# Kernel tuning notes

Hardware: AMD Instinct MI355X
Metric: run time of the kernel (lower is better)

## Reference

```python
import jax, jax.numpy as jnp
import numpy as np

H = 4096   # hidden_dim
I = 4096   # input_dim
V = 32000  # output_size


def setup_inputs() -> dict:
    key = jax.random.key(0)
    ks = jax.random.split(key, 16)
    s_x = 1.0 / np.sqrt(I)
    s_h = 1.0 / np.sqrt(H)
    inp = {
        'prev_h': jax.random.normal(ks[0], (H,), jnp.float32),
        'prev_c': jax.random.normal(ks[1], (H,), jnp.float32),
        'x_t': jax.random.normal(ks[2], (I,), jnp.float32),
        'w_xf': jax.random.normal(ks[3], (H, I), jnp.float32) * s_x,
        'w_hf': jax.random.normal(ks[4], (H, H), jnp.float32) * s_h,
        'b_f': jnp.zeros((H,), jnp.float32),
        'w_xi': jax.random.normal(ks[5], (H, I), jnp.float32) * s_x,
        'w_hi': jax.random.normal(ks[6], (H, H), jnp.float32) * s_h,
        'b_i': jnp.zeros((H,), jnp.float32),
        'w_xg': jax.random.normal(ks[7], (H, I), jnp.float32) * s_x,
        'w_hg': jax.random.normal(ks[8], (H, H), jnp.float32) * s_h,
        'b_g': jnp.zeros((H,), jnp.float32),
        'w_xo': jax.random.normal(ks[9], (H, I), jnp.float32) * s_x,
        'w_ho': jax.random.normal(ks[10], (H, H), jnp.float32) * s_h,
        'b_o': jnp.zeros((H,), jnp.float32),
        'w_hy': jax.random.normal(ks[11], (V, H), jnp.float32) * s_h,
        'b_y': jnp.zeros((V,), jnp.float32),
    }
    return inp


def reference(prev_h, prev_c, x_t,
              w_xf, w_hf, b_f,
              w_xi, w_hi, b_i,
              w_xg, w_hg, b_g,
              w_xo, w_ho, b_o,
              w_hy, b_y):
    # Fuse the 8 small matvecs into 2 stacked matvecs: [4H, I] @ x and [4H, H] @ h.
    W_x = jnp.concatenate([w_xf, w_xi, w_xg, w_xo], axis=0)  # [4H, I]
    W_h = jnp.concatenate([w_hf, w_hi, w_hg, w_ho], axis=0)  # [4H, H]
    b = jnp.concatenate([b_f, b_i, b_g, b_o], axis=0)        # [4H]
    gates = W_x @ x_t + W_h @ prev_h + b                      # [4H]
    f_t = jax.nn.sigmoid(gates[0:H])
    i_t = jax.nn.sigmoid(gates[H:2 * H])
    g_t = jnp.tanh(gates[2 * H:3 * H])
    o_t = jax.nn.sigmoid(gates[3 * H:4 * H])
    c_t = f_t * prev_c + i_t * g_t
    h_t = o_t * jnp.tanh(c_t)
    y_t = jax.nn.softmax(w_hy @ h_t + b_y, axis=-1)           # [V]
    return (h_t, c_t, y_t)
```

## Files before the change

### kernel.cpp

```cpp
#include <hip/hip_runtime.h>
#include <math.h>

#define HDIM 4096
#define VDIM 32000
#define NPART 125

__device__ inline float wave_reduce_sum(float v) {
    #pragma unroll
    for (int off = 32; off > 0; off >>= 1)
        v += __shfl_down(v, off, 64);
    return v;
}

__device__ inline float wave_reduce_max(float v) {
    #pragma unroll
    for (int off = 32; off > 0; off >>= 1)
        v = fmaxf(v, __shfl_down(v, off, 64));
    return v;
}

__global__ __launch_bounds__(256) void lstm_gates_kernel(
    const float* __restrict__ prev_h, const float* __restrict__ prev_c,
    const float* __restrict__ x_t,
    const float* __restrict__ w_xf, const float* __restrict__ w_hf, const float* __restrict__ b_f,
    const float* __restrict__ w_xi, const float* __restrict__ w_hi, const float* __restrict__ b_i,
    const float* __restrict__ w_xg, const float* __restrict__ w_hg, const float* __restrict__ b_g,
    const float* __restrict__ w_xo, const float* __restrict__ w_ho, const float* __restrict__ b_o,
    float* __restrict__ out)
{
    __shared__ float s_x[HDIM];
    __shared__ float s_h[HDIM];
    for (int i = threadIdx.x * 4; i < HDIM; i += 256 * 4) {
        *reinterpret_cast<float4*>(&s_x[i]) = *reinterpret_cast<const float4*>(&x_t[i]);
        *reinterpret_cast<float4*>(&s_h[i]) = *reinterpret_cast<const float4*>(&prev_h[i]);
    }
    __syncthreads();

    const int row  = blockIdx.x;
    const int wave = threadIdx.x >> 6;
    const int lane = threadIdx.x & 63;

    const float* wx; const float* wh; const float* bb;
    if      (wave == 0) { wx = w_xf; wh = w_hf; bb = b_f; }
    else if (wave == 1) { wx = w_xi; wh = w_hi; bb = b_i; }
    else if (wave == 2) { wx = w_xg; wh = w_hg; bb = b_g; }
    else                { wx = w_xo; wh = w_ho; bb = b_o; }
    wx += (size_t)row * HDIM;
    wh += (size_t)row * HDIM;

    float accx = 0.f, acch = 0.f;
    #pragma unroll 4
    for (int j = lane * 4; j < HDIM; j += 64 * 4) {
        float4 a = *reinterpret_cast<const float4*>(wx + j);
        float4 v = *reinterpret_cast<const float4*>(&s_x[j]);
        accx += a.x * v.x + a.y * v.y + a.z * v.z + a.w * v.w;
        float4 b = *reinterpret_cast<const float4*>(wh + j);
        float4 u = *reinterpret_cast<const float4*>(&s_h[j]);
        acch += b.x * u.x + b.y * u.y + b.z * u.z + b.w * u.w;
    }
    float acc = wave_reduce_sum(accx + acch);

    __shared__ float g4[4];
    if (lane == 0) g4[wave] = acc + bb[row];
    __syncthreads();
    if (threadIdx.x == 0) {
        float ft = 1.f / (1.f + expf(-g4[0]));
        float it = 1.f / (1.f + expf(-g4[1]));
        float gt = tanhf(g4[2]);
        float ot = 1.f / (1.f + expf(-g4[3]));
        float c  = ft * prev_c[row] + it * gt;
        float h  = ot * tanhf(c);
        out[row]        = h;
        out[HDIM + row] = c;
    }
}

__global__ __launch_bounds__(256) void logits_kernel(
    const float* __restrict__ w_hy, const float* __restrict__ b_y,
    const float* __restrict__ h, float* __restrict__ logits)
{
    __shared__ float s_h[HDIM];
    for (int i = threadIdx.x * 4; i < HDIM; i += 256 * 4)
        *reinterpret_cast<float4*>(&s_h[i]) = *reinterpret_cast<const float4*>(&h[i]);
    __syncthreads();

    const int row  = blockIdx.x * 4 + (threadIdx.x >> 6);
    const int lane = threadIdx.x & 63;
    const float* w = w_hy + (size_t)row * HDIM;

    float acc0 = 0.f, acc1 = 0.f;
    #pragma unroll 4
    for (int j = lane * 8; j < HDIM; j += 64 * 8) {
        float4 a = *reinterpret_cast<const float4*>(w + j);
        float4 v = *reinterpret_cast<const float4*>(&s_h[j]);
        acc0 += a.x * v.x + a.y * v.y + a.z * v.z + a.w * v.w;
        float4 b = *reinterpret_cast<const float4*>(w + j + 4);
        float4 u = *reinterpret_cast<const float4*>(&s_h[j + 4]);
        acc1 += b.x * u.x + b.y * u.y + b.z * u.z + b.w * u.w;
    }
    float acc = wave_reduce_sum(acc0 + acc1);
    if (lane == 0) logits[row] = acc + b_y[row];
}

__global__ __launch_bounds__(256) void softmax_partial_kernel(
    const float* __restrict__ logits, float2* __restrict__ part)
{
    const int wave = threadIdx.x >> 6;
    const int lane = threadIdx.x & 63;
    float v = logits[blockIdx.x * 256 + threadIdx.x];

    float m = wave_reduce_max(v);
    __shared__ float sm[4];
    if (lane == 0) sm[wave] = m;
    __syncthreads();
    m = fmaxf(fmaxf(sm[0], sm[1]), fmaxf(sm[2], sm[3]));

    float s = wave_reduce_sum(expf(v - m));
    __shared__ float ss[4];
    if (lane == 0) ss[wave] = s;
    __syncthreads();
    if (threadIdx.x == 0)
        part[blockIdx.x] = make_float2(m, ss[0] + ss[1] + ss[2] + ss[3]);
}

__global__ __launch_bounds__(128) void softmax_combine_kernel(
    const float2* __restrict__ part, float* __restrict__ stats)
{
    const int tid = threadIdx.x;
    float2 p = (tid < NPART) ? part[tid] : make_float2(-1e30f, 0.f);

    float m = wave_reduce_max(p.x);
    __shared__ float sm[2];
    if ((tid & 63) == 0) sm[tid >> 6] = m;
    __syncthreads();
    float M = fmaxf(sm[0], sm[1]);

    float s = wave_reduce_sum(p.y * expf(p.x - M));
    __shared__ float s2[2];
    if ((tid & 63) == 0) s2[tid >> 6] = s;
    __syncthreads();
    if (tid == 0) { stats[0] = M; stats[1] = 1.f / (s2[0] + s2[1]); }
}

__global__ __launch_bounds__(256) void softmax_norm_kernel(
    const float* __restrict__ logits, const float* __restrict__ stats,
    float* __restrict__ y)
{
    const int i = blockIdx.x * 256 + threadIdx.x;
    if (i < VDIM) y[i] = expf(logits[i] - stats[0]) * stats[1];
}

extern "C" void kernel_launch(void* const* d_in, const int* in_sizes, int n_in,
                              void* d_out, int out_size, void* d_ws, size_t ws_size,
                              hipStream_t stream)
{
    const float* prev_h = (const float*)d_in[0];
    const float* prev_c = (const float*)d_in[1];
    const float* x_t    = (const float*)d_in[2];
    const float* w_xf   = (const float*)d_in[3];
    const float* w_hf   = (const float*)d_in[4];
    const float* b_f    = (const float*)d_in[5];
    const float* w_xi   = (const float*)d_in[6];
    const float* w_hi   = (const float*)d_in[7];
    const float* b_i    = (const float*)d_in[8];
    const float* w_xg   = (const float*)d_in[9];
    const float* w_hg   = (const float*)d_in[10];
    const float* b_g    = (const float*)d_in[11];
    const float* w_xo   = (const float*)d_in[12];
    const float* w_ho   = (const float*)d_in[13];
    const float* b_o    = (const float*)d_in[14];
    const float* w_hy   = (const float*)d_in[15];
    const float* b_y    = (const float*)d_in[16];

    float* out = (float*)d_out;
    float* h_t = out;
    float* y_t = out + 2 * HDIM;

    float*  logits = (float*)d_ws;
    float*  stats  = logits + VDIM;
    float2* part   = (float2*)(stats + 2);

    lstm_gates_kernel<<<HDIM, 256, 0, stream>>>(
        prev_h, prev_c, x_t,
        w_xf, w_hf, b_f, w_xi, w_hi, b_i,
        w_xg, w_hg, b_g, w_xo, w_ho, b_o, out);

    logits_kernel<<<VDIM / 4, 256, 0, stream>>>(w_hy, b_y, h_t, logits);

    softmax_partial_kernel<<<NPART, 256, 0, stream>>>(logits, part);

    softmax_combine_kernel<<<1, 128, 0, stream>>>(part, stats);

    softmax_norm_kernel<<<(VDIM + 255) / 256, 256, 0, stream>>>(logits, stats, y_t);
}
```

Before: 190.4 us.

## Process four rows per wave, fuse softmax partials into logits, use nontemporal loads

Both matvec kernels now have each wave compute four rows instead of one, so each shared-memory vector load is reused across four weight rows, and the block count drops accordingly. Weight loads use nontemporal hints because the matrices are streamed once. The per-block softmax max/sum partial is computed inside the logits kernel, which removes the separate partial kernel and its reread of the logits. The combine stage becomes one 1024-thread block using an online max/sum over 2000 partials, and the normalize kernel is vectorized to float4. The risks are fewer resident waves and a longer serial combine.

```diff
diff --git a/kernel.cpp b/kernel.cpp
--- a/kernel.cpp
+++ b/kernel.cpp
@@ -3,7 +3,10 @@
 
 #define HDIM 4096
 #define VDIM 32000
-#define NPART 125
+#define GBLK (HDIM / 4)
+#define LBLK (VDIM / 16)
+
+typedef float floatx4 __attribute__((ext_vector_type(4)));
 
 __device__ inline float wave_reduce_sum(float v) {
     #pragma unroll
@@ -12,11 +15,12 @@
     return v;
 }
 
-__device__ inline float wave_reduce_max(float v) {
-    #pragma unroll
-    for (int off = 32; off > 0; off >>= 1)
-        v = fmaxf(v, __shfl_down(v, off, 64));
-    return v;
+__device__ inline floatx4 ntload4(const float* p) {
+    return __builtin_nontemporal_load(reinterpret_cast<const floatx4*>(p));
+}
+
+__device__ inline float dot4(floatx4 a, floatx4 b) {
+    return a.x * b.x + a.y * b.y + a.z * b.z + a.w * b.w;
 }
 
 __global__ __launch_bounds__(256) void lstm_gates_kernel(
@@ -30,44 +34,50 @@
 {
     __shared__ float s_x[HDIM];
     __shared__ float s_h[HDIM];
+    __shared__ float sg[4][4];
     for (int i = threadIdx.x * 4; i < HDIM; i += 256 * 4) {
         *reinterpret_cast<float4*>(&s_x[i]) = *reinterpret_cast<const float4*>(&x_t[i]);
         *reinterpret_cast<float4*>(&s_h[i]) = *reinterpret_cast<const float4*>(&prev_h[i]);
     }
     __syncthreads();
 
-    const int row  = blockIdx.x;
     const int wave = threadIdx.x >> 6;
     const int lane = threadIdx.x & 63;
+    const int row0 = blockIdx.x * 4;
 
     const float* wx; const float* wh; const float* bb;
     if      (wave == 0) { wx = w_xf; wh = w_hf; bb = b_f; }
     else if (wave == 1) { wx = w_xi; wh = w_hi; bb = b_i; }
     else if (wave == 2) { wx = w_xg; wh = w_hg; bb = b_g; }
     else                { wx = w_xo; wh = w_ho; bb = b_o; }
-    wx += (size_t)row * HDIM;
-    wh += (size_t)row * HDIM;
-
-    float accx = 0.f, acch = 0.f;
-    #pragma unroll 4
+    wx += (size_t)row0 * HDIM;
+    wh += (size_t)row0 * HDIM;
+
+    float acc[4] = {0.f, 0.f, 0.f, 0.f};
     for (int j = lane * 4; j < HDIM; j += 64 * 4) {
-        float4 a = *reinterpret_cast<const float4*>(wx + j);
-        float4 v = *reinterpret_cast<const float4*>(&s_x[j]);
-        accx += a.x * v.x + a.y * v.y + a.z * v.z + a.w * v.w;
-        float4 b = *reinterpret_cast<const float4*>(wh + j);
-        float4 u = *reinterpret_cast<const float4*>(&s_h[j]);
-        acch += b.x * u.x + b.y * u.y + b.z * u.z + b.w * u.w;
-    }
-    float acc = wave_reduce_sum(accx + acch);
-
-    __shared__ float g4[4];
-    if (lane == 0) g4[wave] = acc + bb[row];
-    __syncthreads();
-    if (threadIdx.x == 0) {
-        float ft = 1.f / (1.f + expf(-g4[0]));
-        float it = 1.f / (1.f + expf(-g4[1]));
-        float gt = tanhf(g4[2]);
-        float ot = 1.f / (1.f + expf(-g4[3]));
+        floatx4 v = *reinterpret_cast<const floatx4*>(&s_x[j]);
+        floatx4 u = *reinterpret_cast<const floatx4*>(&s_h[j]);
+        #pragma unroll
+        for (int r = 0; r < 4; ++r) {
+            floatx4 a = ntload4(wx + (size_t)r * HDIM + j);
+            floatx4 b = ntload4(wh + (size_t)r * HDIM + j);
+            acc[r] += dot4(a, v) + dot4(b, u);
+        }
+    }
+    #pragma unroll
+    for (int r = 0; r < 4; ++r) {
+        float s = wave_reduce_sum(acc[r]);
+        if (lane == 0) sg[wave][r] = s + bb[row0 + r];
+    }
+    __syncthreads();
+
+    if (threadIdx.x < 4) {
+        const int r   = threadIdx.x;
+        const int row = row0 + r;
+        float ft = 1.f / (1.f + expf(-sg[0][r]));
+        float it = 1.f / (1.f + expf(-sg[1][r]));
+        float gt = tanhf(sg[2][r]);
+        float ot = 1.f / (1.f + expf(-sg[3][r]));
         float c  = ft * prev_c[row] + it * gt;
         float h  = ot * tanhf(c);
         out[row]        = h;
@@ -77,77 +87,110 @@
 
 __global__ __launch_bounds__(256) void logits_kernel(
     const float* __restrict__ w_hy, const float* __restrict__ b_y,
-    const float* __restrict__ h, float* __restrict__ logits)
+    const float* __restrict__ h, float* __restrict__ logits,
+    float2* __restrict__ part)
 {
     __shared__ float s_h[HDIM];
+    __shared__ float sl[16];
     for (int i = threadIdx.x * 4; i < HDIM; i += 256 * 4)
         *reinterpret_cast<float4*>(&s_h[i]) = *reinterpret_cast<const float4*>(&h[i]);
     __syncthreads();
 
-    const int row  = blockIdx.x * 4 + (threadIdx.x >> 6);
-    const int lane = threadIdx.x & 63;
-    const float* w = w_hy + (size_t)row * HDIM;
-
-    float acc0 = 0.f, acc1 = 0.f;
-    #pragma unroll 4
-    for (int j = lane * 8; j < HDIM; j += 64 * 8) {
-        float4 a = *reinterpret_cast<const float4*>(w + j);
-        float4 v = *reinterpret_cast<const float4*>(&s_h[j]);
-        acc0 += a.x * v.x + a.y * v.y + a.z * v.z + a.w * v.w;
-        float4 b = *reinterpret_cast<const float4*>(w + j + 4);
-        float4 u = *reinterpret_cast<const float4*>(&s_h[j + 4]);
-        acc1 += b.x * u.x + b.y * u.y + b.z * u.z + b.w * u.w;
-    }
-    float acc = wave_reduce_sum(acc0 + acc1);
-    if (lane == 0) logits[row] = acc + b_y[row];
-}
-
-__global__ __launch_bounds__(256) void softmax_partial_kernel(
-    const float* __restrict__ logits, float2* __restrict__ part)
-{
     const int wave = threadIdx.x >> 6;
     const int lane = threadIdx.x & 63;
-    float v = logits[blockIdx.x * 256 + threadIdx.x];
-
-    float m = wave_reduce_max(v);
-    __shared__ float sm[4];
-    if (lane == 0) sm[wave] = m;
-    __syncthreads();
-    m = fmaxf(fmaxf(sm[0], sm[1]), fmaxf(sm[2], sm[3]));
-
-    float s = wave_reduce_sum(expf(v - m));
-    __shared__ float ss[4];
-    if (lane == 0) ss[wave] = s;
-    __syncthreads();
-    if (threadIdx.x == 0)
-        part[blockIdx.x] = make_float2(m, ss[0] + ss[1] + ss[2] + ss[3]);
-}
-
-__global__ __launch_bounds__(128) void softmax_combine_kernel(
+    const int row0 = blockIdx.x * 16 + wave * 4;
+    const float* w = w_hy + (size_t)row0 * HDIM;
+
+    float acc[4] = {0.f, 0.f, 0.f, 0.f};
+    for (int j = lane * 4; j < HDIM; j += 64 * 4) {
+        floatx4 u = *reinterpret_cast<const floatx4*>(&s_h[j]);
+        #pragma unroll
+        for (int r = 0; r < 4; ++r) {
+            floatx4 a = ntload4(w + (size_t)r * HDIM + j);
+            acc[r] += dot4(a, u);
+        }
+    }
+    #pragma unroll
+    for (int r = 0; r < 4; ++r) {
+        float s = wave_reduce_sum(acc[r]);
+        if (lane == 0) {
+            float lv = s + b_y[row0 + r];
+            logits[row0 + r] = lv;
+            sl[wave * 4 + r] = lv;
+        }
+    }
+    __syncthreads();
+
+    if (threadIdx.x < 16) {
+        float v = sl[threadIdx.x];
+        float m = v;
+        #pragma unroll
+        for (int off = 8; off > 0; off >>= 1)
+            m = fmaxf(m, __shfl_xor(m, off, 64));
+        float e = expf(v - m);
+        #pragma unroll
+        for (int off = 8; off > 0; off >>= 1)
+            e += __shfl_xor(e, off, 64);
+        if (threadIdx.x == 0) part[blockIdx.x] = make_float2(m, e);
+    }
+}
+
+__global__ __launch_bounds__(1024) void softmax_combine_kernel(
     const float2* __restrict__ part, float* __restrict__ stats)
 {
-    const int tid = threadIdx.x;
-    float2 p = (tid < NPART) ? part[tid] : make_float2(-1e30f, 0.f);
-
-    float m = wave_reduce_max(p.x);
-    __shared__ float sm[2];
-    if ((tid & 63) == 0) sm[tid >> 6] = m;
-    __syncthreads();
-    float M = fmaxf(sm[0], sm[1]);
-
-    float s = wave_reduce_sum(p.y * expf(p.x - M));
-    __shared__ float s2[2];
-    if ((tid & 63) == 0) s2[tid >> 6] = s;
-    __syncthreads();
-    if (tid == 0) { stats[0] = M; stats[1] = 1.f / (s2[0] + s2[1]); }
+    const int tid  = threadIdx.x;
+    const int wave = tid >> 6;
+    const int lane = tid & 63;
+
+    float m = -1e30f, s = 0.f;
+    for (int i = tid; i < LBLK; i += 1024) {
+        float2 p = part[i];
+        if (p.x > m) { s = s * expf(m - p.x) + p.y; m = p.x; }
+        else         { s += p.y * expf(p.x - m); }
+    }
+
+    __shared__ float sm[16];
+    float mm = m;
+    #pragma unroll
+    for (int off = 32; off > 0; off >>= 1)
+        mm = fmaxf(mm, __shfl_xor(mm, off, 64));
+    if (lane == 0) sm[wave] = mm;
+    __syncthreads();
+    float M = sm[0];
+    #pragma unroll
+    for (int i = 1; i < 16; ++i) M = fmaxf(M, sm[i]);
+
+    float sc = s * expf(m - M);
+    #pragma unroll
+    for (int off = 32; off > 0; off >>= 1)
+        sc += __shfl_xor(sc, off, 64);
+    __shared__ float ss[16];
+    if (lane == 0) ss[wave] = sc;
+    __syncthreads();
+    if (tid == 0) {
+        float S = 0.f;
+        #pragma unroll
+        for (int i = 0; i < 16; ++i) S += ss[i];
+        stats[0] = M;
+        stats[1] = 1.f / S;
+    }
 }
 
 __global__ __launch_bounds__(256) void softmax_norm_kernel(
     const float* __restrict__ logits, const float* __restrict__ stats,
     float* __restrict__ y)
 {
-    const int i = blockIdx.x * 256 + threadIdx.x;
-    if (i < VDIM) y[i] = expf(logits[i] - stats[0]) * stats[1];
+    const int idx = blockIdx.x * 256 + threadIdx.x;
+    if (idx < VDIM / 4) {
+        float  M = stats[0], R = stats[1];
+        float4 l = *reinterpret_cast<const float4*>(logits + idx * 4);
+        float4 o;
+        o.x = expf(l.x - M) * R;
+        o.y = expf(l.y - M) * R;
+        o.z = expf(l.z - M) * R;
+        o.w = expf(l.w - M) * R;
+        *reinterpret_cast<float4*>(y + idx * 4) = o;
+    }
 }
 
 extern "C" void kernel_launch(void* const* d_in, const int* in_sizes, int n_in,
@@ -180,16 +223,14 @@
     float*  stats  = logits + VDIM;
     float2* part   = (float2*)(stats + 2);
 
-    lstm_gates_kernel<<<HDIM, 256, 0, stream>>>(
+    lstm_gates_kernel<<<GBLK, 256, 0, stream>>>(
         prev_h, prev_c, x_t,
         w_xf, w_hf, b_f, w_xi, w_hi, b_i,
         w_xg, w_hg, b_g, w_xo, w_ho, b_o, out);
 
-    logits_kernel<<<VDIM / 4, 256, 0, stream>>>(w_hy, b_y, h_t, logits);
-
-    softmax_partial_kernel<<<NPART, 256, 0, stream>>>(logits, part);
-
-    softmax_combine_kernel<<<1, 128, 0, stream>>>(part, stats);
-
-    softmax_norm_kernel<<<(VDIM + 255) / 256, 256, 0, stream>>>(logits, stats, y_t);
-}
+    logits_kernel<<<LBLK, 256, 0, stream>>>(w_hy, b_y, h_t, logits, part);
+
+    softmax_combine_kernel<<<1, 1024, 0, stream>>>(part, stats);
+
+    softmax_norm_kernel<<<(VDIM / 4 + 255) / 256, 256, 0, stream>>>(logits, stats, y_t);
+}
```

Result: no change. 186.9 us, median of 2 (-1.8%).
